# Kernel tuning notes

Measured on AMD Instinct MI355X. Metric: run time of the kernel, lower is better.

Reference implementation:

```python
import jax, jax.numpy as jnp
import numpy as np

K = 3
UP_H, UP_W = 120, 160  # up_size
RES_H, RES_W = UP_H + K - 1, UP_W + K - 1  # bilinear target before valid depthwise conv


def _bilinear_align_corners(x, out_h, out_w):
    """PyTorch UpsamplingBilinear2d (align_corners=True). x: [B,C,H,W]."""
    B, C, H, W = x.shape
    # row interpolation
    hy = jnp.arange(out_h, dtype=x.dtype) * ((H - 1) / (out_h - 1))
    y0 = jnp.floor(hy).astype(jnp.int32)
    y1 = jnp.minimum(y0 + 1, H - 1)
    fy = (hy - y0.astype(x.dtype))[None, None, :, None]
    x = x[:, :, y0, :] * (1 - fy) + x[:, :, y1, :] * fy  # [B,C,out_h,W]
    # col interpolation
    wx = jnp.arange(out_w, dtype=x.dtype) * ((W - 1) / (out_w - 1))
    x0i = jnp.floor(wx).astype(jnp.int32)
    x1i = jnp.minimum(x0i + 1, W - 1)
    fx = (wx - x0i.astype(x.dtype))[None, None, None, :]
    return x[:, :, :, x0i] * (1 - fx) + x[:, :, :, x1i] * fx  # [B,C,out_h,out_w]


def setup_inputs() -> dict:
    key = jax.random.key(0)
    k1, k2, k3 = jax.random.split(key, 3)
    C_in, C_out = 256, 128
    x = jax.random.normal(k1, (8, C_in, 60, 80), dtype=jnp.float32)
    # depthwise kernel [C_in, 1, K, K], pointwise [C_out, C_in]; fan-in-ish scale
    w_dw = jax.random.normal(k2, (C_in, 1, K, K), dtype=jnp.float32) * (1.0 / K)
    w_pw = jax.random.normal(k3, (C_out, C_in), dtype=jnp.float32) * (1.0 / np.sqrt(C_in))
    return {"x": x, "w_dw": w_dw, "w_pw": w_pw}


def reference(x, w_dw, w_pw):
    C_in = x.shape[1]
    # 1) bilinear upsample (align_corners=True) to (UP_H+K-1, UP_W+K-1)
    up = _bilinear_align_corners(x, RES_H, RES_W)
    # 2) depthwise KxK conv, stride 1, VALID padding -> [B,C_in,UP_H,UP_W]
    dw = jax.lax.conv_general_dilated(
        up, w_dw, window_strides=(1, 1), padding="VALID",
        dimension_numbers=("NCHW", "OIHW", "NCHW"),
        feature_group_count=C_in)
    # 3) pointwise 1x1 conv -> [B,C_out,UP_H,UP_W]
    return jnp.einsum("bchw,oc->bohw", dw, w_pw)
```

## Files before the change

kernel.cpp:

```cpp
#include <hip/hip_runtime.h>

#define CIN  256
#define HIN  60
#define WIN  80
#define UPH  120
#define UPW  160
#define COUT 128
#define NPIX (UPH*UPW)

typedef __bf16 bf16x2 __attribute__((ext_vector_type(2)));
typedef __bf16 bf16x8 __attribute__((ext_vector_type(8)));
typedef float  floatx4 __attribute__((ext_vector_type(4)));

#define A_NT 320
#define A_XR 5
#define A_CP 17
#define A_AS 49

__global__ __launch_bounds__(A_NT, 5) void dw_kernel(
    const float* __restrict__ x,
    const float* __restrict__ wdw,
    __bf16* __restrict__ dwb,
    int b0)
{
    __shared__ bf16x2 s_px[A_XR * 84 * A_CP];
    __shared__ float  s_A[16 * A_AS];

    const int tid = threadIdx.x;
    const int h0  = blockIdx.x * 4;
    const int cb  = blockIdx.y * 16;
    const int bl  = blockIdx.z;
    const int b   = b0 + bl;

    const float HS = 59.0f / 121.0f;
    const float WS = 79.0f / 161.0f;
    const int rbase = (int)(h0 * HS);

    const float* xb = x + ((size_t)b * CIN + cb) * (HIN * WIN);
    #pragma unroll
    for (int k = 0; k < 6; k++) {
        int i = tid + k * A_NT;
        if (i < 1680) {
            int ch  = i / 105;
            int rem = i - ch * 105;
            int r   = rem / 21;
            int c4  = rem - r * 21;
            int gy  = min(rbase + r, HIN - 1);
            const float* xrow = xb + (size_t)ch * (HIN * WIN) + gy * WIN;
            int base = (r * 84 + c4 * 4) * A_CP + ch;
            if (c4 < 20) {
                float4 v = *(const float4*)(xrow + c4 * 4);
                float x5 = xrow[min(c4 * 4 + 4, WIN - 1)];
                s_px[base]          = (bf16x2){(__bf16)v.x, (__bf16)v.y};
                s_px[base + A_CP]   = (bf16x2){(__bf16)v.y, (__bf16)v.z};
                s_px[base + 2*A_CP] = (bf16x2){(__bf16)v.z, (__bf16)v.w};
                s_px[base + 3*A_CP] = (bf16x2){(__bf16)v.w, (__bf16)x5};
            } else {
                float v = xrow[WIN - 1];
                bf16x2 p = {(__bf16)v, (__bf16)v};
                s_px[base]          = p;
                s_px[base + A_CP]   = p;
                s_px[base + 2*A_CP] = p;
                s_px[base + 3*A_CP] = p;
            }
        }
    }
    for (int i = tid; i < 16 * 4 * 9; i += A_NT) {
        int ch  = i / 36;
        int rem = i - ch * 36;
        int h   = rem / 9;
        int dyj = rem - h * 9;
        int dy  = dyj / 3;
        int j   = dyj - dy * 3;
        int ybh = (int)((h0 + h) * HS);
        float acc = 0.f;
        #pragma unroll
        for (int i3 = 0; i3 < 3; i3++) {
            float hy = (h0 + h + i3) * HS;
            int y0 = (int)hy;
            float fy = hy - (float)y0;
            int y1 = min(y0 + 1, HIN - 1);
            float wgt = ((y0 - ybh) == dy ? (1.f - fy) : 0.f)
                      + ((y1 - ybh) == dy ? fy : 0.f);
            acc = fmaf(wgt, wdw[(cb + ch) * 9 + i3 * 3 + j], acc);
        }
        s_A[ch * A_AS + h * 12 + dy * 4 + j] = acc;
    }
    __syncthreads();

    const int ch  = tid & 15;
    const int rid = tid >> 4;
    const int wq  = rid * 8;
    int rbh[4];
    #pragma unroll
    for (int hh = 0; hh < 4; hh++)
        rbh[hh] = (int)((h0 + hh) * HS) - rbase;

    float fx[10]; int wi[10];
    #pragma unroll
    for (int j = 0; j < 10; j++) {
        float wx = (float)(wq + j) * WS;
        int x0 = (int)wx;
        fx[j] = wx - (float)x0;
        wi[j] = x0 * A_CP + ch;
    }

    float d[4][8];
    #pragma unroll
    for (int hh = 0; hh < 4; hh++)
        #pragma unroll
        for (int i = 0; i < 8; i++) d[hh][i] = 0.f;

    #pragma unroll
    for (int r = 0; r < A_XR; r++) {
        float cx[10];
        #pragma unroll
        for (int j = 0; j < 10; j++) {
            bf16x2 p = s_px[r * 84 * A_CP + wi[j]];
            float lo = (float)p[0], hi = (float)p[1];
            cx[j] = fmaf(fx[j], hi - lo, lo);
        }
        #pragma unroll
        for (int hh = 0; hh < 4; hh++) {
            int dyL = r - rbh[hh];
            if ((unsigned)dyL <= 2u) {
                const float* Ab = &s_A[ch * A_AS + hh * 12 + dyL * 4];
                float A0 = Ab[0], A1 = Ab[1], A2 = Ab[2];
                #pragma unroll
                for (int i = 0; i < 8; i++)
                    d[hh][i] = fmaf(A0, cx[i],
                               fmaf(A1, cx[i+1],
                               fmaf(A2, cx[i+2], d[hh][i])));
            }
        }
    }
    #pragma unroll
    for (int hh = 0; hh < 4; hh++) {
        bf16x8 o;
        #pragma unroll
        for (int i = 0; i < 8; i++) o[i] = (__bf16)d[hh][i];
        size_t off = ((size_t)bl * CIN + cb + ch) * NPIX
                   + (size_t)(h0 + hh) * UPW + wq;
        *(bf16x8*)(dwb + off) = o;
    }
}

#define B_NT 512
#define B_WS 264
#define B_DS 40

__global__ __launch_bounds__(B_NT, 4) void pw_kernel(
    const __bf16* __restrict__ dwb,
    const float* __restrict__ wpw,
    float* __restrict__ out,
    int b0)
{
    __shared__ __align__(16) __bf16 s_wpw[COUT * B_WS];
    __shared__ __align__(16) __bf16 s_dw[128 * B_DS];

    const int tid  = threadIdx.x;
    const int tile = blockIdx.x;
    const int bl   = blockIdx.y;
    const int b    = b0 + bl;

    {
        const int o = tid >> 2, seg = tid & 3;
        #pragma unroll
        for (int q = 0; q < 8; q++) {
            int c0 = seg * 64 + q * 8;
            float4 v0 = *(const float4*)(wpw + (size_t)o * CIN + c0);
            float4 v1 = *(const float4*)(wpw + (size_t)o * CIN + c0 + 4);
            bf16x8 f = {(__bf16)v0.x, (__bf16)v0.y, (__bf16)v0.z, (__bf16)v0.w,
                        (__bf16)v1.x, (__bf16)v1.y, (__bf16)v1.z, (__bf16)v1.w};
            *(bf16x8*)&s_wpw[o * B_WS + c0] = f;
        }
    }

    const int wave = tid >> 6, lane = tid & 63;
    const int quad = lane >> 4, l16 = lane & 15;
    const int o32  = (wave & 3) * 32;
    const int pg   = wave >> 2;

    floatx4 acc[2][4];
    #pragma unroll
    for (int a = 0; a < 2; a++)
        #pragma unroll
        for (int p = 0; p < 4; p++) acc[a][p] = (floatx4){0.f,0.f,0.f,0.f};

    const __bf16* dwbase = dwb + (size_t)bl * CIN * NPIX + tile * 128;
    const int cS = tid & 31, p8 = tid >> 5;

    bf16x8 v = *(const bf16x8*)(dwbase + (size_t)cS * NPIX + p8 * 8);

    for (int ck = 0; ck < 8; ck++) {
        __syncthreads();
        #pragma unroll
        for (int i = 0; i < 8; i++)
            s_dw[(p8 * 8 + i) * B_DS + cS] = v[i];
        __syncthreads();

        if (ck < 7)
            v = *(const bf16x8*)(dwbase + (size_t)((ck+1) * 32 + cS) * NPIX + p8 * 8);

        bf16x8 af0 = *(const bf16x8*)&s_wpw[(o32 + l16) * B_WS + ck * 32 + quad * 8];
        bf16x8 af1 = *(const bf16x8*)&s_wpw[(o32 + 16 + l16) * B_WS + ck * 32 + quad * 8];
        #pragma unroll
        for (int pt = 0; pt < 4; pt++) {
            bf16x8 bf = *(const bf16x8*)&s_dw[(pg * 64 + pt * 16 + l16) * B_DS + quad * 8];
            acc[0][pt] = __builtin_amdgcn_mfma_f32_16x16x32_bf16(af0, bf, acc[0][pt], 0, 0, 0);
            acc[1][pt] = __builtin_amdgcn_mfma_f32_16x16x32_bf16(af1, bf, acc[1][pt], 0, 0, 0);
        }
    }

    float* ob = out + (size_t)b * COUT * NPIX + tile * 128;
    #pragma unroll
    for (int ot = 0; ot < 2; ot++)
        #pragma unroll
        for (int pt = 0; pt < 4; pt++)
            #pragma unroll
            for (int r = 0; r < 4; r++)
                ob[(size_t)(o32 + ot * 16 + quad * 4 + r) * NPIX
                   + pg * 64 + pt * 16 + l16] = acc[ot][pt][r];
}

extern "C" void kernel_launch(void* const* d_in, const int* in_sizes, int n_in,
                              void* d_out, int out_size, void* d_ws, size_t ws_size,
                              hipStream_t stream) {
    const float* x   = (const float*)d_in[0];
    const float* wdw = (const float*)d_in[1];
    const float* wpw = (const float*)d_in[2];
    float* out = (float*)d_out;
    __bf16* dwb = (__bf16*)d_ws;

    int bs = 8;
    while (bs > 1 && (size_t)bs * CIN * NPIX * 2 > ws_size) bs >>= 1;

    for (int b0 = 0; b0 < 8; b0 += bs) {
        dim3 gA(30, CIN / 16, bs);
        dw_kernel<<<gA, A_NT, 0, stream>>>(x, wdw, dwb, b0);
        dim3 gB(NPIX / 128, bs);
        pw_kernel<<<gB, B_NT, 0, stream>>>(dwb, wpw, out, b0);
    }
}
```

Measured before the change: 202.9 us.

## Store depthwise intermediate pixel-major and feed MFMA directly from global memory

The depthwise kernel now processes 32 channels per block, packs channel pairs into 32-bit bf16 words, and transposes its output through shared memory. It writes the intermediate in pixel-major (NHWC) order with channels contiguous. The pointwise kernel then reads MFMA B-fragments straight from global memory and converts weights from fp32 registers on the fly, so its shared-memory staging, transpose and barriers go away. The cost is uncached 16-byte strided global reads in the GEMM, repeated weight loads per block, and lower occupancy for the depthwise kernel.

```diff
diff --git a/kernel.cpp b/kernel.cpp
--- a/kernel.cpp
+++ b/kernel.cpp
@@ -6,29 +6,35 @@
 #define UPH  120
 #define UPW  160
 #define COUT 128
-#define NPIX (UPH*UPW)
-
-typedef __bf16 bf16x2 __attribute__((ext_vector_type(2)));
+#define NPIX 19200
+
 typedef __bf16 bf16x8 __attribute__((ext_vector_type(8)));
 typedef float  floatx4 __attribute__((ext_vector_type(4)));
 
-#define A_NT 320
-#define A_XR 5
-#define A_CP 17
-#define A_AS 49
-
-__global__ __launch_bounds__(A_NT, 5) void dw_kernel(
+__device__ inline uint32_t pack_bf2(float lo, float hi) {
+    union { __bf16 h; unsigned short s; } a, b;
+    a.h = (__bf16)lo; b.h = (__bf16)hi;
+    return (uint32_t)a.s | ((uint32_t)b.s << 16);
+}
+__device__ inline float unp_lo(uint32_t w) { return __uint_as_float(w << 16); }
+__device__ inline float unp_hi(uint32_t w) { return __uint_as_float(w & 0xFFFF0000u); }
+
+#define A_NT  320
+#define A_SOS 20
+
+__global__ __launch_bounds__(A_NT, 3) void dw_kernel(
     const float* __restrict__ x,
     const float* __restrict__ wdw,
     __bf16* __restrict__ dwb,
     int b0)
 {
-    __shared__ bf16x2 s_px[A_XR * 84 * A_CP];
-    __shared__ float  s_A[16 * A_AS];
+    __shared__ uint32_t s_px[5 * 16 * 84];
+    __shared__ float    s_A[32 * 49];
+    __shared__ uint32_t s_out[160 * A_SOS];
 
     const int tid = threadIdx.x;
     const int h0  = blockIdx.x * 4;
-    const int cb  = blockIdx.y * 16;
+    const int cb  = blockIdx.y * 32;
     const int bl  = blockIdx.z;
     const int b   = b0 + bl;
 
@@ -36,36 +42,30 @@
     const float WS = 79.0f / 161.0f;
     const int rbase = (int)(h0 * HS);
 
-    const float* xb = x + ((size_t)b * CIN + cb) * (HIN * WIN);
-    #pragma unroll
-    for (int k = 0; k < 6; k++) {
-        int i = tid + k * A_NT;
-        if (i < 1680) {
-            int ch  = i / 105;
-            int rem = i - ch * 105;
-            int r   = rem / 21;
-            int c4  = rem - r * 21;
-            int gy  = min(rbase + r, HIN - 1);
-            const float* xrow = xb + (size_t)ch * (HIN * WIN) + gy * WIN;
-            int base = (r * 84 + c4 * 4) * A_CP + ch;
-            if (c4 < 20) {
-                float4 v = *(const float4*)(xrow + c4 * 4);
-                float x5 = xrow[min(c4 * 4 + 4, WIN - 1)];
-                s_px[base]          = (bf16x2){(__bf16)v.x, (__bf16)v.y};
-                s_px[base + A_CP]   = (bf16x2){(__bf16)v.y, (__bf16)v.z};
-                s_px[base + 2*A_CP] = (bf16x2){(__bf16)v.z, (__bf16)v.w};
-                s_px[base + 3*A_CP] = (bf16x2){(__bf16)v.w, (__bf16)x5};
-            } else {
-                float v = xrow[WIN - 1];
-                bf16x2 p = {(__bf16)v, (__bf16)v};
-                s_px[base]          = p;
-                s_px[base + A_CP]   = p;
-                s_px[base + 2*A_CP] = p;
-                s_px[base + 3*A_CP] = p;
-            }
-        }
-    }
-    for (int i = tid; i < 16 * 4 * 9; i += A_NT) {
+    {
+        const int u = tid >> 2;
+        const int part = tid & 3;
+        const int chp_s = u / 5;
+        const int r_s = u - chp_s * 5;
+        const int gy = min(rbase + r_s, HIN - 1);
+        const float* r0 = x + ((size_t)(b * CIN + cb + 2 * chp_s)) * (HIN * WIN)
+                            + gy * WIN + part * 20;
+        const float* r1 = r0 + HIN * WIN;
+        uint32_t* dst = &s_px[(r_s * 16 + chp_s) * 84 + part * 20];
+        float l0 = 0.f, l1 = 0.f;
+        #pragma unroll
+        for (int q = 0; q < 5; q++) {
+            float4 v0 = *(const float4*)(r0 + q * 4);
+            float4 v1 = *(const float4*)(r1 + q * 4);
+            dst[q * 4 + 0] = pack_bf2(v0.x, v1.x);
+            dst[q * 4 + 1] = pack_bf2(v0.y, v1.y);
+            dst[q * 4 + 2] = pack_bf2(v0.z, v1.z);
+            dst[q * 4 + 3] = pack_bf2(v0.w, v1.w);
+            l0 = v0.w; l1 = v1.w;
+        }
+        if (part == 3) dst[20] = pack_bf2(l0, l1);
+    }
+    for (int i = tid; i < 32 * 4 * 9; i += A_NT) {
         int ch  = i / 36;
         int rem = i - ch * 36;
         int h   = rem / 9;
@@ -84,98 +84,96 @@
                       + ((y1 - ybh) == dy ? fy : 0.f);
             acc = fmaf(wgt, wdw[(cb + ch) * 9 + i3 * 3 + j], acc);
         }
-        s_A[ch * A_AS + h * 12 + dy * 4 + j] = acc;
+        s_A[ch * 49 + h * 12 + dy * 4 + j] = acc;
     }
     __syncthreads();
 
-    const int ch  = tid & 15;
-    const int rid = tid >> 4;
-    const int wq  = rid * 8;
-    int rbh[4];
-    #pragma unroll
-    for (int hh = 0; hh < 4; hh++)
-        rbh[hh] = (int)((h0 + hh) * HS) - rbase;
-
-    float fx[10]; int wi[10];
+    const int chp = tid / 20;
+    const int run = tid - chp * 20;
+    const int wq  = run * 8;
+
+    int x0i[10]; float fx[10];
     #pragma unroll
     for (int j = 0; j < 10; j++) {
         float wx = (float)(wq + j) * WS;
         int x0 = (int)wx;
-        fx[j] = wx - (float)x0;
-        wi[j] = x0 * A_CP + ch;
-    }
-
-    float d[4][8];
+        fx[j]  = wx - (float)x0;
+        x0i[j] = x0;
+    }
+    int rbh[4];
     #pragma unroll
     for (int hh = 0; hh < 4; hh++)
-        #pragma unroll
-        for (int i = 0; i < 8; i++) d[hh][i] = 0.f;
-
-    #pragma unroll
-    for (int r = 0; r < A_XR; r++) {
-        float cx[10];
+        rbh[hh] = (int)((h0 + hh) * HS) - rbase;
+
+    float d0[4][8], d1[4][8];
+    #pragma unroll
+    for (int hh = 0; hh < 4; hh++)
+        #pragma unroll
+        for (int i = 0; i < 8; i++) { d0[hh][i] = 0.f; d1[hh][i] = 0.f; }
+
+    #pragma unroll
+    for (int r = 0; r < 5; r++) {
+        const uint32_t* rowp = &s_px[(r * 16 + chp) * 84];
+        float cx0[10], cx1[10];
         #pragma unroll
         for (int j = 0; j < 10; j++) {
-            bf16x2 p = s_px[r * 84 * A_CP + wi[j]];
-            float lo = (float)p[0], hi = (float)p[1];
-            cx[j] = fmaf(fx[j], hi - lo, lo);
+            uint32_t wa = rowp[x0i[j]];
+            uint32_t wb = rowp[x0i[j] + 1];
+            float a0 = unp_lo(wa), a1 = unp_lo(wb);
+            float b0_ = unp_hi(wa), b1_ = unp_hi(wb);
+            cx0[j] = fmaf(fx[j], a1 - a0, a0);
+            cx1[j] = fmaf(fx[j], b1_ - b0_, b0_);
         }
         #pragma unroll
         for (int hh = 0; hh < 4; hh++) {
             int dyL = r - rbh[hh];
             if ((unsigned)dyL <= 2u) {
-                const float* Ab = &s_A[ch * A_AS + hh * 12 + dyL * 4];
-                float A0 = Ab[0], A1 = Ab[1], A2 = Ab[2];
+                const float* Aa = &s_A[(2 * chp) * 49 + hh * 12 + dyL * 4];
+                const float* Ab = &s_A[(2 * chp + 1) * 49 + hh * 12 + dyL * 4];
+                float a0 = Aa[0], a1 = Aa[1], a2 = Aa[2];
+                float e0 = Ab[0], e1 = Ab[1], e2 = Ab[2];
                 #pragma unroll
-                for (int i = 0; i < 8; i++)
-                    d[hh][i] = fmaf(A0, cx[i],
-                               fmaf(A1, cx[i+1],
-                               fmaf(A2, cx[i+2], d[hh][i])));
+                for (int i = 0; i < 8; i++) {
+                    d0[hh][i] = fmaf(a0, cx0[i],
+                                fmaf(a1, cx0[i+1],
+                                fmaf(a2, cx0[i+2], d0[hh][i])));
+                    d1[hh][i] = fmaf(e0, cx1[i],
+                                fmaf(e1, cx1[i+1],
+                                fmaf(e2, cx1[i+2], d1[hh][i])));
+                }
             }
         }
     }
+
+    const int pxl  = tid >> 1;
+    const int half = tid & 1;
     #pragma unroll
     for (int hh = 0; hh < 4; hh++) {
-        bf16x8 o;
-        #pragma unroll
-        for (int i = 0; i < 8; i++) o[i] = (__bf16)d[hh][i];
-        size_t off = ((size_t)bl * CIN + cb + ch) * NPIX
-                   + (size_t)(h0 + hh) * UPW + wq;
-        *(bf16x8*)(dwb + off) = o;
-    }
-}
-
-#define B_NT 512
-#define B_WS 264
-#define B_DS 40
-
-__global__ __launch_bounds__(B_NT, 4) void pw_kernel(
+        __syncthreads();
+        #pragma unroll
+        for (int i = 0; i < 8; i++)
+            s_out[(wq + i) * A_SOS + chp] = pack_bf2(d0[hh][i], d1[hh][i]);
+        __syncthreads();
+        uint4 v0 = *(const uint4*)&s_out[pxl * A_SOS + half * 8];
+        uint4 v1 = *(const uint4*)&s_out[pxl * A_SOS + half * 8 + 4];
+        size_t gpx = (size_t)bl * NPIX + (size_t)(h0 + hh) * UPW + pxl;
+        uint32_t* gdst = (uint32_t*)(dwb + gpx * CIN + cb) + half * 8;
+        *(uint4*)gdst       = v0;
+        *(uint4*)(gdst + 4) = v1;
+    }
+}
+
+__global__ __launch_bounds__(512, 4) void pw_kernel(
     const __bf16* __restrict__ dwb,
     const float* __restrict__ wpw,
     float* __restrict__ out,
     int b0)
 {
-    __shared__ __align__(16) __bf16 s_wpw[COUT * B_WS];
-    __shared__ __align__(16) __bf16 s_dw[128 * B_DS];
-
     const int tid  = threadIdx.x;
     const int tile = blockIdx.x;
     const int bl   = blockIdx.y;
     const int b    = b0 + bl;
 
-    {
-        const int o = tid >> 2, seg = tid & 3;
-        #pragma unroll
-        for (int q = 0; q < 8; q++) {
-            int c0 = seg * 64 + q * 8;
-            float4 v0 = *(const float4*)(wpw + (size_t)o * CIN + c0);
-            float4 v1 = *(const float4*)(wpw + (size_t)o * CIN + c0 + 4);
-            bf16x8 f = {(__bf16)v0.x, (__bf16)v0.y, (__bf16)v0.z, (__bf16)v0.w,
-                        (__bf16)v1.x, (__bf16)v1.y, (__bf16)v1.z, (__bf16)v1.w};
-            *(bf16x8*)&s_wpw[o * B_WS + c0] = f;
-        }
-    }
-
     const int wave = tid >> 6, lane = tid & 63;
     const int quad = lane >> 4, l16 = lane & 15;
     const int o32  = (wave & 3) * 32;
@@ -187,32 +185,36 @@
         #pragma unroll
         for (int p = 0; p < 4; p++) acc[a][p] = (floatx4){0.f,0.f,0.f,0.f};
 
-    const __bf16* dwbase = dwb + (size_t)bl * CIN * NPIX + tile * 128;
-    const int cS = tid & 31, p8 = tid >> 5;
-
-    bf16x8 v = *(const bf16x8*)(dwbase + (size_t)cS * NPIX + p8 * 8);
-
+    const int pxb = tile * 128 + pg * 64;
+    const __bf16* dwp = dwb + ((size_t)bl * NPIX + pxb) * CIN;
+    const float* w0p = wpw + (size_t)(o32 + l16) * CIN + quad * 8;
+    const float* w1p = w0p + 16 * CIN;
+
+    #define LOAD_AF(dst, base, ck) { \
+        float4 u = *(const float4*)((base) + (ck) * 32); \
+        float4 v = *(const float4*)((base) + (ck) * 32 + 4); \
+        dst = (bf16x8){(__bf16)u.x,(__bf16)u.y,(__bf16)u.z,(__bf16)u.w, \
+                       (__bf16)v.x,(__bf16)v.y,(__bf16)v.z,(__bf16)v.w}; }
+
+    bf16x8 af0, af1;
+    LOAD_AF(af0, w0p, 0);
+    LOAD_AF(af1, w1p, 0);
+
+    #pragma unroll
     for (int ck = 0; ck < 8; ck++) {
-        __syncthreads();
-        #pragma unroll
-        for (int i = 0; i < 8; i++)
-            s_dw[(p8 * 8 + i) * B_DS + cS] = v[i];
-        __syncthreads();
-
-        if (ck < 7)
-            v = *(const bf16x8*)(dwbase + (size_t)((ck+1) * 32 + cS) * NPIX + p8 * 8);
-
-        bf16x8 af0 = *(const bf16x8*)&s_wpw[(o32 + l16) * B_WS + ck * 32 + quad * 8];
-        bf16x8 af1 = *(const bf16x8*)&s_wpw[(o32 + 16 + l16) * B_WS + ck * 32 + quad * 8];
+        bf16x8 nf0, nf1;
+        if (ck < 7) { LOAD_AF(nf0, w0p, ck + 1); LOAD_AF(nf1, w1p, ck + 1); }
         #pragma unroll
         for (int pt = 0; pt < 4; pt++) {
-            bf16x8 bf = *(const bf16x8*)&s_dw[(pg * 64 + pt * 16 + l16) * B_DS + quad * 8];
+            bf16x8 bf = *(const bf16x8*)(dwp + (size_t)(pt * 16 + l16) * CIN
+                                             + ck * 32 + quad * 8);
             acc[0][pt] = __builtin_amdgcn_mfma_f32_16x16x32_bf16(af0, bf, acc[0][pt], 0, 0, 0);
             acc[1][pt] = __builtin_amdgcn_mfma_f32_16x16x32_bf16(af1, bf, acc[1][pt], 0, 0, 0);
         }
-    }
-
-    float* ob = out + (size_t)b * COUT * NPIX + tile * 128;
+        af0 = nf0; af1 = nf1;
+    }
+
+    float* ob = out + (size_t)b * COUT * NPIX + pxb;
     #pragma unroll
     for (int ot = 0; ot < 2; ot++)
         #pragma unroll
@@ -220,7 +222,7 @@
             #pragma unroll
             for (int r = 0; r < 4; r++)
                 ob[(size_t)(o32 + ot * 16 + quad * 4 + r) * NPIX
-                   + pg * 64 + pt * 16 + l16] = acc[ot][pt][r];
+                   + pt * 16 + l16] = acc[ot][pt][r];
 }
 
 extern "C" void kernel_launch(void* const* d_in, const int* in_sizes, int n_in,
@@ -236,9 +238,9 @@
     while (bs > 1 && (size_t)bs * CIN * NPIX * 2 > ws_size) bs >>= 1;
 
     for (int b0 = 0; b0 < 8; b0 += bs) {
-        dim3 gA(30, CIN / 16, bs);
+        dim3 gA(30, CIN / 32, bs);
         dw_kernel<<<gA, A_NT, 0, stream>>>(x, wdw, dwb, b0);
         dim3 gB(NPIX / 128, bs);
-        pw_kernel<<<gB, B_NT, 0, stream>>>(dwb, wpw, out, b0);
-    }
-}
+        pw_kernel<<<gB, 512, 0, stream>>>(dwb, wpw, out, b0);
+    }
+}
```

Measured after the change: 312.3 us. +53.9%, slower.
